# Kernel optimization log

Measured on AMD Instinct MI355X. Metric: run time of the kernel, lower is better.

The kernel has to match this reference:

```python
import jax, jax.numpy as jnp
import numpy as np

H = 1024
N_IN = 128
N_OUT = 128
B = 64
S = 512


def _rnn_layer(x, W_ih, b_ih, W_hh, b_hh):
    # PyTorch nn.RNN (tanh): h_t = tanh(x_t @ W_ih^T + b_ih + h_{t-1} @ W_hh^T + b_hh)
    # Precompute the input projection for all timesteps (one big GEMM),
    # then scan only the recurrent GEMM.
    xp = jnp.einsum('bsi,hi->bsh', x, W_ih) + b_ih + b_hh  # [B,S,H]

    def step(h, xt):
        h_new = jnp.tanh(xt + h @ W_hh.T)
        return h_new, h_new

    h0 = jnp.zeros((x.shape[0], W_hh.shape[0]), x.dtype)
    _, hs = jax.lax.scan(step, h0, jnp.swapaxes(xp, 0, 1))  # [S,B,H]
    return jnp.swapaxes(hs, 0, 1)  # [B,S,H]


def setup_inputs() -> dict:
    key = jax.random.key(0)
    ks = jax.random.split(key, 11)
    s = 1.0 / np.sqrt(H)  # matches PyTorch uniform(-1/sqrt(H), 1/sqrt(H)) scale
    return {
        'x': jax.random.normal(ks[0], (B, S, N_IN), jnp.float32),
        'W_ih0': jax.random.normal(ks[1], (H, N_IN), jnp.float32) * s,
        'b_ih0': jax.random.normal(ks[2], (H,), jnp.float32) * s,
        'W_hh0': jax.random.normal(ks[3], (H, H), jnp.float32) * s,
        'b_hh0': jax.random.normal(ks[4], (H,), jnp.float32) * s,
        'W_ih1': jax.random.normal(ks[5], (H, H), jnp.float32) * s,
        'b_ih1': jax.random.normal(ks[6], (H,), jnp.float32) * s,
        'W_hh1': jax.random.normal(ks[7], (H, H), jnp.float32) * s,
        'b_hh1': jax.random.normal(ks[8], (H,), jnp.float32) * s,
        'W_fc': jax.random.normal(ks[9], (N_OUT, H), jnp.float32) * s,
        'b_fc': jax.random.normal(ks[10], (N_OUT,), jnp.float32) * s,
    }


def reference(x, W_ih0, b_ih0, W_hh0, b_hh0, W_ih1, b_ih1, W_hh1, b_hh1, W_fc, b_fc):
    h = _rnn_layer(x, W_ih0, b_ih0, W_hh0, b_hh0)   # layer 0
    h = _rnn_layer(h, W_ih1, b_ih1, W_hh1, b_hh1)   # layer 1
    last = h[:, -1, :]                               # take final timestep [B,H]
    return last @ W_fc.T + b_fc                      # [B,N_OUT]
```

## Files before the change

### kernel.cpp

```cpp
#include <hip/hip_runtime.h>
#include <hip/hip_fp16.h>

#define H     1024
#define NIN   128
#define NOUT  128
#define BATCH 64
#define SEQ   512
#define MROWS (BATCH * SEQ)

typedef _Float16 half8  __attribute__((ext_vector_type(8)));
typedef _Float16 half4v __attribute__((ext_vector_type(4)));
typedef float    f32x4  __attribute__((ext_vector_type(4)));
typedef unsigned uint4v __attribute__((ext_vector_type(4)));
typedef unsigned long long u64;

__global__ void cvt16_kernel(const float* __restrict__ src,
                             _Float16* __restrict__ dst, int n4) {
  int i = blockIdx.x * blockDim.x + threadIdx.x;
  if (i < n4) {
    float4 v = reinterpret_cast<const float4*>(src)[i];
    half4v h = {(_Float16)v.x, (_Float16)v.y, (_Float16)v.z, (_Float16)v.w};
    *reinterpret_cast<half4v*>(dst + (size_t)i * 4) = h;
  }
}

__global__ void init_misc_kernel(const float* __restrict__ b_ih0,
                                 const float* __restrict__ b_hh0,
                                 const float* __restrict__ b_ih1,
                                 const float* __restrict__ b_hh1,
                                 float* __restrict__ bias0,
                                 float* __restrict__ bias1,
                                 unsigned* __restrict__ zero_base,
                                 int zero_words) {
  int i = blockIdx.x * blockDim.x + threadIdx.x;
  if (i < H) {
    bias0[i] = b_ih0[i] + b_hh0[i];
    bias1[i] = b_ih1[i] + b_hh1[i];
  }
  for (int j = i; j < zero_words; j += gridDim.x * blockDim.x) zero_base[j] = 0u;
}

__global__ __launch_bounds__(256) void gemm_f16_kernel(
    const _Float16* __restrict__ A, const _Float16* __restrict__ B,
    const float* __restrict__ bias, float* __restrict__ C,
    int M, int N, int K) {
  __shared__ _Float16 As[128][40];
  __shared__ _Float16 Bs[128][40];
  const int m0 = blockIdx.x * 128;
  const int n0 = blockIdx.y * 128;
  const int tid = threadIdx.x;
  const int wave = tid >> 6, lane = tid & 63;
  const int wm = (wave >> 1) * 64, wn = (wave & 1) * 64;
  const int fr = lane & 15;
  const int kg = (lane >> 4) * 8;

  f32x4 acc[4][4] = {};
  for (int k0 = 0; k0 < K; k0 += 32) {
    __syncthreads();
    for (int c = tid; c < 512; c += 256) {
      int row = c >> 2, ko = (c & 3) * 8;
      *reinterpret_cast<half8*>(&As[row][ko]) =
          *reinterpret_cast<const half8*>(&A[(size_t)(m0 + row) * K + k0 + ko]);
      *reinterpret_cast<half8*>(&Bs[row][ko]) =
          *reinterpret_cast<const half8*>(&B[(size_t)(n0 + row) * K + k0 + ko]);
    }
    __syncthreads();
    half8 af[4], bf[4];
#pragma unroll
    for (int i = 0; i < 4; ++i)
      af[i] = *reinterpret_cast<const half8*>(&As[wm + i * 16 + fr][kg]);
#pragma unroll
    for (int j = 0; j < 4; ++j)
      bf[j] = *reinterpret_cast<const half8*>(&Bs[wn + j * 16 + fr][kg]);
#pragma unroll
    for (int i = 0; i < 4; ++i)
#pragma unroll
      for (int j = 0; j < 4; ++j)
        acc[i][j] = __builtin_amdgcn_mfma_f32_16x16x32_f16(af[i], bf[j],
                                                           acc[i][j], 0, 0, 0);
  }
  const int lr = (lane >> 4) * 4, lc = lane & 15;
#pragma unroll
  for (int j = 0; j < 4; ++j) {
    int n = n0 + wn + j * 16 + lc;
    float bn = bias ? bias[n] : 0.0f;
#pragma unroll
    for (int i = 0; i < 4; ++i) {
      int m = m0 + wm + i * 16 + lr;
#pragma unroll
      for (int r = 0; r < 4; ++r)
        C[(size_t)(m + r) * N + n] = acc[i][j][r] + bn;
    }
  }
}

#define NCLUST 16
#define CWGS   16
#define GB     4
#define UNITS  2048

__global__ __launch_bounds__(256, 1) void scan_kernel(
    const float* __restrict__ xp,
    const _Float16* __restrict__ W16,
    u64* __restrict__ fastbuf,
    u64* __restrict__ slowbuf,
    _Float16* __restrict__ hs_out,
    float* __restrict__ h_last)
{
  __shared__ unsigned lds_h[2][UNITS];

  const int blk = blockIdx.x;
  const int cluster = blk & (NCLUST - 1);
  const int rank = blk >> 4;
  const int tid = threadIdx.x;
  const int wave = tid >> 6;
  const int lane = tid & 63;
  const int fr = lane & 15;
  const int g = lane >> 4;
  const int kg8 = g * 8;
  const int wcol = rank * 64 + wave * 16;
  const int c0 = wcol + g * 4;
  const int rb = lane & 15;
  const bool act = rb < GB;

  f32x4 wfrag[32];
#pragma unroll
  for (int kt = 0; kt < 32; ++kt) {
    wfrag[kt] = *reinterpret_cast<const f32x4*>(
        &W16[(size_t)(wcol + fr) * H + kt * 32 + kg8]);
    asm volatile("" : "+v"(wfrag[kt]));
  }

  u64* fcl = fastbuf + (size_t)cluster * (2 * UNITS);
  u64* scl = slowbuf + (size_t)cluster * (2 * UNITS);
  const int b0 = cluster * GB;

  const int w0 = (c0 >> 5) * 64 + rb * 16 + (((c0 >> 3) & 3) << 2) +
                 ((c0 >> 1) & 3);

  float4 xpv = {0.f, 0.f, 0.f, 0.f};
  if (act)
    xpv = *reinterpret_cast<const float4*>(
        &xp[((size_t)(b0 + rb) * SEQ + 0) * H + c0]);

  for (int t = 0; t < SEQ; ++t) {
    uint4v q0, q1, q2, q3;
    if (t > 0) {
      const char* fb = (const char*)(fcl + (t & 1) * UNITS) + (size_t)tid * 16;
      const char* sb = (const char*)(scl + (t & 1) * UNITS) + (size_t)tid * 16;
      const unsigned tag = (unsigned)t;
      int it = 0;
      while (true) {
        if (it < 4) {
          asm volatile(
              "global_load_dwordx4 %0, %4, off sc0 nt\n\t"
              "global_load_dwordx4 %1, %5, off sc0 nt\n\t"
              "global_load_dwordx4 %2, %6, off sc0 nt\n\t"
              "global_load_dwordx4 %3, %7, off sc0 nt\n\t"
              "s_waitcnt vmcnt(0)"
              : "=&v"(q0), "=&v"(q1), "=&v"(q2), "=&v"(q3)
              : "v"(fb), "v"(fb + 4096), "v"(fb + 8192), "v"(fb + 12288)
              : "memory");
        } else {
          asm volatile(
              "global_load_dwordx4 %0, %4, off sc0 sc1\n\t"
              "global_load_dwordx4 %1, %5, off sc0 sc1\n\t"
              "global_load_dwordx4 %2, %6, off sc0 sc1\n\t"
              "global_load_dwordx4 %3, %7, off sc0 sc1\n\t"
              "s_waitcnt vmcnt(0)"
              : "=&v"(q0), "=&v"(q1), "=&v"(q2), "=&v"(q3)
              : "v"(sb), "v"(sb + 4096), "v"(sb + 8192), "v"(sb + 12288)
              : "memory");
        }
        bool ok = (q0.y == tag) & (q0.w == tag) & (q1.y == tag) &
                  (q1.w == tag) & (q2.y == tag) & (q2.w == tag) &
                  (q3.y == tag) & (q3.w == tag);
        if (__ballot(ok) == ~0ull) break;
        ++it;
        if (it > 4) __builtin_amdgcn_s_sleep(1);
      }
    }

    float4 xpn = {0.f, 0.f, 0.f, 0.f};
    {
      int t2 = (t + 1 < SEQ) ? (t + 1) : (SEQ - 1);
      if (act)
        xpn = *reinterpret_cast<const float4*>(
            &xp[((size_t)(b0 + rb) * SEQ + t2) * H + c0]);
    }

    f32x4 s = {0.f, 0.f, 0.f, 0.f};
    if (t > 0) {
      unsigned* lb_w = lds_h[t & 1];
#pragma unroll
      for (int j = 0; j < 4; ++j) {
        uint4v q = (j == 0) ? q0 : (j == 1) ? q1 : (j == 2) ? q2 : q3;
        u64 pk = (u64)q.x | ((u64)q.z << 32);
        *reinterpret_cast<u64*>(&lb_w[tid * 2 + j * 512]) = pk;
      }
      __syncthreads();

      const char* lb = reinterpret_cast<const char*>(lds_h[t & 1]);
      f32x4 acc[4] = {{0.f, 0.f, 0.f, 0.f}, {0.f, 0.f, 0.f, 0.f},
                      {0.f, 0.f, 0.f, 0.f}, {0.f, 0.f, 0.f, 0.f}};
#pragma unroll
      for (int kt = 0; kt < 32; ++kt) {
        half8 hf = *reinterpret_cast<const half8*>(
            lb + kt * 256 + (rb & 3) * 64 + g * 16);
        acc[kt & 3] = __builtin_amdgcn_mfma_f32_16x16x32_f16(
            __builtin_bit_cast(half8, wfrag[kt]), hf, acc[kt & 3], 0, 0, 0);
      }
      s = (acc[0] + acc[1]) + (acc[2] + acc[3]);
    }

    if (act) {
      union { u64 u; _Float16 h[4]; unsigned w[2]; } pk;
      float hv[4];
#pragma unroll
      for (int r = 0; r < 4; ++r) {
        float v = s[r] + xpv[r];
        v = fminf(fmaxf(v, -15.f), 15.f);
        float e = __expf(2.f * v);
        hv[r] = 1.f - 2.f * __builtin_amdgcn_rcpf(e + 1.f);
        pk.h[r] = (_Float16)hv[r];
      }
      if (t < SEQ - 1) {
        const unsigned tagw = (unsigned)(t + 1);
        uint4v sv = {pk.w[0], tagw, pk.w[1], tagw};
        u64* fdst = fcl + ((t + 1) & 1) * UNITS + w0;
        u64* sdst = scl + ((t + 1) & 1) * UNITS + w0;
        asm volatile(
            "global_store_dwordx4 %0, %2, off sc0\n\t"
            "global_store_dwordx4 %1, %2, off sc0 sc1"
            :: "v"(fdst), "v"(sdst), "v"(sv)
            : "memory");
      }
      if (hs_out) {
        *reinterpret_cast<u64*>(
            &hs_out[((size_t)(b0 + rb) * SEQ + t) * H + c0]) = pk.u;
      } else if (t == SEQ - 1) {
        float4 o = {hv[0], hv[1], hv[2], hv[3]};
        *reinterpret_cast<float4*>(&h_last[(size_t)(b0 + rb) * H + c0]) = o;
      }
    }
    xpv = xpn;
  }
}

__global__ __launch_bounds__(256) void fc_kernel(
    const float* __restrict__ h_last, const float* __restrict__ W_fc,
    const float* __restrict__ b_fc, float* __restrict__ out) {
  const int wave = threadIdx.x >> 6, lane = threadIdx.x & 63;
  const int o = blockIdx.x * 4 + wave;
  const int b = o >> 7, n = o & 127;
  const float* hr = h_last + (size_t)b * H;
  const float* wr = W_fc + (size_t)n * H;
  float s = 0.0f;
  for (int k = lane; k < H; k += 64) s += hr[k] * wr[k];
#pragma unroll
  for (int off = 32; off; off >>= 1) s += __shfl_down(s, off);
  if (lane == 0) out[o] = s + b_fc[n];
}

extern "C" void kernel_launch(void* const* d_in, const int* in_sizes, int n_in,
                              void* d_out, int out_size, void* d_ws,
                              size_t ws_size, hipStream_t stream) {
  (void)in_sizes; (void)n_in; (void)out_size; (void)ws_size;
  const float* x     = (const float*)d_in[0];
  const float* W_ih0 = (const float*)d_in[1];
  const float* b_ih0 = (const float*)d_in[2];
  const float* W_hh0 = (const float*)d_in[3];
  const float* b_hh0 = (const float*)d_in[4];
  const float* W_ih1 = (const float*)d_in[5];
  const float* b_ih1 = (const float*)d_in[6];
  const float* W_hh1 = (const float*)d_in[7];
  const float* b_hh1 = (const float*)d_in[8];
  const float* W_fc  = (const float*)d_in[9];
  const float* b_fc  = (const float*)d_in[10];
  float* out = (float*)d_out;

  char* ws = (char*)d_ws;
  size_t off = 0;
  auto carve = [&](size_t bytes) {
    char* p = ws + off;
    off += (bytes + 255) & ~(size_t)255;
    return p;
  };
  float*    xpbuf   = (float*)   carve((size_t)MROWS * H * 4);
  _Float16* hs0_16  = (_Float16*)carve((size_t)MROWS * H * 2);
  _Float16* x16     = (_Float16*)carve((size_t)MROWS * NIN * 2);
  _Float16* wih0_16 = (_Float16*)carve((size_t)H * NIN * 2);
  _Float16* whh0_16 = (_Float16*)carve((size_t)H * H * 2);
  _Float16* wih1_16 = (_Float16*)carve((size_t)H * H * 2);
  _Float16* whh1_16 = (_Float16*)carve((size_t)H * H * 2);
  float*    bias0   = (float*)   carve(H * 4);
  float*    bias1   = (float*)   carve(H * 4);
  const size_t RING = (size_t)NCLUST * 2 * UNITS * 8;
  u64*      fb0     = (u64*)     carve(RING);
  u64*      fb1     = (u64*)     carve(RING);
  u64*      sb0     = (u64*)     carve(RING);
  u64*      sb1     = (u64*)     carve(RING);
  float*    h_lastp = (float*)   carve((size_t)BATCH * H * 4);

  const int zero_words = (int)(RING * 4 / 4);

  init_misc_kernel<<<(zero_words + 255) / 256, 256, 0, stream>>>(
      b_ih0, b_hh0, b_ih1, b_hh1, bias0, bias1, (unsigned*)fb0, zero_words);

  cvt16_kernel<<<(MROWS * NIN / 4 + 255) / 256, 256, 0, stream>>>(x, x16,
                                                                  MROWS * NIN / 4);
  cvt16_kernel<<<(H * NIN / 4 + 255) / 256, 256, 0, stream>>>(W_ih0, wih0_16,
                                                              H * NIN / 4);
  cvt16_kernel<<<(H * H / 4 + 255) / 256, 256, 0, stream>>>(W_hh0, whh0_16,
                                                            H * H / 4);
  cvt16_kernel<<<(H * H / 4 + 255) / 256, 256, 0, stream>>>(W_ih1, wih1_16,
                                                            H * H / 4);
  cvt16_kernel<<<(H * H / 4 + 255) / 256, 256, 0, stream>>>(W_hh1, whh1_16,
                                                            H * H / 4);

  {
    dim3 grid(MROWS / 128, H / 128);
    gemm_f16_kernel<<<grid, 256, 0, stream>>>(x16, wih0_16, bias0, xpbuf,
                                              MROWS, H, NIN);
  }

  {
    const float* xp_p = xpbuf; const _Float16* w_p = whh0_16;
    u64* fb_p = fb0; u64* sb_p = sb0;
    _Float16* hs_p = hs0_16; float* hl_p = nullptr;
    void* args[] = {&xp_p, &w_p, &fb_p, &sb_p, &hs_p, &hl_p};
    hipLaunchCooperativeKernel((const void*)scan_kernel, dim3(256), dim3(256),
                               args, 0, stream);
  }

  {
    dim3 grid(MROWS / 128, H / 128);
    gemm_f16_kernel<<<grid, 256, 0, stream>>>(hs0_16, wih1_16, bias1, xpbuf,
                                              MROWS, H, H);
  }

  {
    const float* xp_p = xpbuf; const _Float16* w_p = whh1_16;
    u64* fb_p = fb1; u64* sb_p = sb1;
    _Float16* hs_p = nullptr; float* hl_p = h_lastp;
    void* args[] = {&xp_p, &w_p, &fb_p, &sb_p, &hs_p, &hl_p};
    hipLaunchCooperativeKernel((const void*)scan_kernel, dim3(256), dim3(256),
                               args, 0, stream);
  }

  fc_kernel<<<BATCH * NOUT / 4, 256, 0, stream>>>(h_lastp, W_fc, b_fc, out);
}
```

Before: 1.990 ms.

## Drop redundant slow-path stores and fall back to slow buffer adaptively

The scan kernel previously wrote each hidden-state fragment to both a fast (sc0) and a slow (sc0 sc1, system-coherent) exchange buffer every timestep. It now writes only the fast buffer and polls it up to a fixed iteration count with plain sc0 loads (the nt hint is dropped). If a workgroup fails to see the data in that window, it copies its slice of the fast buffer into the slow buffer and switches itself and its workgroup into a mode that writes and polls the slow path. The aim is to remove the per-step extra coherent store and its traffic. The price is a more complex protocol whose correctness depends on the fallback copy and on mode propagation across workgroups in a cluster.

```diff
diff --git a/kernel.cpp b/kernel.cpp
--- a/kernel.cpp
+++ b/kernel.cpp
@@ -94,10 +94,10 @@
   }
 }
 
-#define NCLUST 16
-#define CWGS   16
-#define GB     4
-#define UNITS  2048
+#define NCLUST  16
+#define GB      4
+#define UNITS   2048
+#define F_ITERS 24
 
 __global__ __launch_bounds__(256, 1) void scan_kernel(
     const float* __restrict__ xp,
@@ -108,6 +108,7 @@
     float* __restrict__ h_last)
 {
   __shared__ unsigned lds_h[2][UNITS];
+  __shared__ int lds_mode;
 
   const int blk = blockIdx.x;
   const int cluster = blk & (NCLUST - 1);
@@ -123,6 +124,8 @@
   const int rb = lane & 15;
   const bool act = rb < GB;
 
+  if (tid == 0) lds_mode = 0;
+
   f32x4 wfrag[32];
 #pragma unroll
   for (int kt = 0; kt < 32; ++kt) {
@@ -130,6 +133,7 @@
         &W16[(size_t)(wcol + fr) * H + kt * 32 + kg8]);
     asm volatile("" : "+v"(wfrag[kt]));
   }
+  __syncthreads();
 
   u64* fcl = fastbuf + (size_t)cluster * (2 * UNITS);
   u64* scl = slowbuf + (size_t)cluster * (2 * UNITS);
@@ -137,6 +141,8 @@
 
   const int w0 = (c0 >> 5) * 64 + rb * 16 + (((c0 >> 3) & 3) << 2) +
                  ((c0 >> 1) & 3);
+
+  bool mode = false;
 
   float4 xpv = {0.f, 0.f, 0.f, 0.f};
   if (act)
@@ -146,22 +152,49 @@
   for (int t = 0; t < SEQ; ++t) {
     uint4v q0, q1, q2, q3;
     if (t > 0) {
-      const char* fb = (const char*)(fcl + (t & 1) * UNITS) + (size_t)tid * 16;
-      const char* sb = (const char*)(scl + (t & 1) * UNITS) + (size_t)tid * 16;
       const unsigned tag = (unsigned)t;
-      int it = 0;
-      while (true) {
-        if (it < 4) {
+      const char* fb = (const char*)(fcl + (size_t)(t & 1) * UNITS) +
+                       (size_t)tid * 16;
+      const char* sb = (const char*)(scl + (size_t)(t & 1) * UNITS) +
+                       (size_t)tid * 16;
+      bool got = false;
+      if (!mode) {
+        for (int it = 0; it < F_ITERS; ++it) {
           asm volatile(
-              "global_load_dwordx4 %0, %4, off sc0 nt\n\t"
-              "global_load_dwordx4 %1, %5, off sc0 nt\n\t"
-              "global_load_dwordx4 %2, %6, off sc0 nt\n\t"
-              "global_load_dwordx4 %3, %7, off sc0 nt\n\t"
+              "global_load_dwordx4 %0, %4, off sc0\n\t"
+              "global_load_dwordx4 %1, %5, off sc0\n\t"
+              "global_load_dwordx4 %2, %6, off sc0\n\t"
+              "global_load_dwordx4 %3, %7, off sc0\n\t"
               "s_waitcnt vmcnt(0)"
               : "=&v"(q0), "=&v"(q1), "=&v"(q2), "=&v"(q3)
               : "v"(fb), "v"(fb + 4096), "v"(fb + 8192), "v"(fb + 12288)
               : "memory");
-        } else {
+          bool ok = (q0.y == tag) & (q0.w == tag) & (q1.y == tag) &
+                    (q1.w == tag) & (q2.y == tag) & (q2.w == tag) &
+                    (q3.y == tag) & (q3.w == tag);
+          if (__ballot(ok) == ~0ull) { got = true; break; }
+        }
+        if (!got) {
+          const int base = 128 * rank + lane * 2;
+#pragma unroll
+          for (int s2 = 0; s2 < 2; ++s2) {
+            uint4v d;
+            const u64* srcp = fcl + (size_t)s2 * UNITS + base;
+            u64* dstp = scl + (size_t)s2 * UNITS + base;
+            asm volatile(
+                "global_load_dwordx4 %0, %1, off sc0\n\t"
+                "s_waitcnt vmcnt(0)"
+                : "=&v"(d) : "v"(srcp) : "memory");
+            asm volatile("global_store_dwordx4 %0, %1, off sc0 sc1"
+                         :: "v"(dstp), "v"(d) : "memory");
+          }
+          asm volatile("s_waitcnt vmcnt(0)" ::: "memory");
+          if (lane == 0) lds_mode = 1;
+          mode = true;
+        }
+      }
+      if (!got) {
+        while (true) {
           asm volatile(
               "global_load_dwordx4 %0, %4, off sc0 sc1\n\t"
               "global_load_dwordx4 %1, %5, off sc0 sc1\n\t"
@@ -171,13 +204,12 @@
               : "=&v"(q0), "=&v"(q1), "=&v"(q2), "=&v"(q3)
               : "v"(sb), "v"(sb + 4096), "v"(sb + 8192), "v"(sb + 12288)
               : "memory");
+          bool ok = (q0.y == tag) & (q0.w == tag) & (q1.y == tag) &
+                    (q1.w == tag) & (q2.y == tag) & (q2.w == tag) &
+                    (q3.y == tag) & (q3.w == tag);
+          if (__ballot(ok) == ~0ull) break;
+          __builtin_amdgcn_s_sleep(2);
         }
-        bool ok = (q0.y == tag) & (q0.w == tag) & (q1.y == tag) &
-                  (q1.w == tag) & (q2.y == tag) & (q2.w == tag) &
-                  (q3.y == tag) & (q3.w == tag);
-        if (__ballot(ok) == ~0ull) break;
-        ++it;
-        if (it > 4) __builtin_amdgcn_s_sleep(1);
       }
     }
 
@@ -199,6 +231,7 @@
         *reinterpret_cast<u64*>(&lb_w[tid * 2 + j * 512]) = pk;
       }
       __syncthreads();
+      mode = mode | (lds_mode != 0);
 
       const char* lb = reinterpret_cast<const char*>(lds_h[t & 1]);
       f32x4 acc[4] = {{0.f, 0.f, 0.f, 0.f}, {0.f, 0.f, 0.f, 0.f},
@@ -228,12 +261,16 @@
         const unsigned tagw = (unsigned)(t + 1);
         uint4v sv = {pk.w[0], tagw, pk.w[1], tagw};
         u64* fdst = fcl + ((t + 1) & 1) * UNITS + w0;
-        u64* sdst = scl + ((t + 1) & 1) * UNITS + w0;
-        asm volatile(
-            "global_store_dwordx4 %0, %2, off sc0\n\t"
-            "global_store_dwordx4 %1, %2, off sc0 sc1"
-            :: "v"(fdst), "v"(sdst), "v"(sv)
-            : "memory");
+        if (!mode) {
+          asm volatile("global_store_dwordx4 %0, %1, off sc0"
+                       :: "v"(fdst), "v"(sv) : "memory");
+        } else {
+          u64* sdst = scl + ((t + 1) & 1) * UNITS + w0;
+          asm volatile(
+              "global_store_dwordx4 %0, %2, off sc0\n\t"
+              "global_store_dwordx4 %1, %2, off sc0 sc1"
+              :: "v"(fdst), "v"(sdst), "v"(sv) : "memory");
+        }
       }
       if (hs_out) {
         *reinterpret_cast<u64*>(
```

Result: slower. 2.056 ms (+3.3%).
